# Performance work log

Hardware: AMD Instinct MI355X
Metric: run time of the kernel (lower is better)

Reference implementation:

```python
import jax, jax.numpy as jnp
import numpy as np
from jax import lax

THRESHOLD = 1.0  # threshold_potential from __init__
STRIDE = (1, 1)
PADDING = 'SAME'


def setup_inputs() -> dict:
    key = jax.random.key(0)
    k1, k2, k3 = jax.random.split(key, 3)
    input_to_layer = jax.random.normal(k1, (1, 512, 512, 16), dtype=jnp.float32)
    weights = jax.random.normal(k2, (3, 3, 16, 64), dtype=jnp.float32)
    old_potentials = jax.random.normal(k3, (1, 512, 512, 64), dtype=jnp.float32)
    return {
        'input_to_layer': input_to_layer,
        'weights': weights,
        'old_potentials': old_potentials,
    }


def reference(input_to_layer, weights, old_potentials):
    # conv2d NHWC x HWIO -> NHWC, SAME padding, stride 1 (as tf.nn.conv2d)
    out_conv = lax.conv_general_dilated(
        input_to_layer, weights,
        window_strides=STRIDE, padding=PADDING,
        dimension_numbers=('NHWC', 'HWIO', 'NHWC'))
    # accumulate membrane potential, fused threshold -> spike + reset
    new_potentials = out_conv + old_potentials
    spiked = new_potentials >= THRESHOLD
    curr_spikes = spiked.astype(new_potentials.dtype)
    new_potentials = jnp.where(spiked, 0.0, new_potentials)
    # original returns spikes; new_potentials is the updated state
    return curr_spikes, new_potentials
```

## Files before the change

### kernel.cpp

```cpp
#include <hip/hip_runtime.h>


#define H 512
#define W 512
#define CI 16
#define CO 64
#define TX 32
#define TY 4
#define XT 34
#define YT 6
#define PIX_US 24
#define KS 152
#define SW_CHUNKS ((CO * KS * 2) / 16)

typedef float v4f __attribute__((ext_vector_type(4)));
typedef float f32x4 __attribute__((ext_vector_type(4)));
typedef short short8 __attribute__((ext_vector_type(8)));
typedef unsigned int uint4v __attribute__((ext_vector_type(4)));

__device__ __forceinline__ unsigned int pack2bf(float f0, float f1) {
    unsigned u0 = __builtin_bit_cast(unsigned, f0);
    unsigned u1 = __builtin_bit_cast(unsigned, f1);
    u0 = (u0 + 0x7FFFu + ((u0 >> 16) & 1u)) >> 16;
    u1 = (u1 + 0x7FFFu + ((u1 >> 16) & 1u)) >> 16;
    return u0 | (u1 << 16);
}

__global__ void snn_pack_w(const float* __restrict__ w,
                           unsigned int* __restrict__ wsu)
{
    const int tid = threadIdx.x;
    const int n  = tid & 63;
    const int kq = tid >> 6;
    #pragma unroll
    for (int kk = 0; kk < 18; ++kk) {
        const int k = kq * 36 + kk * 2;
        const float f0 = w[k * CO + n];
        const float f1 = w[(k + 1) * CO + n];
        wsu[(n * KS + k) >> 1] = pack2bf(f0, f1);
    }
    if (kq == 3) {
        #pragma unroll
        for (int i = 0; i < 4; ++i)
            wsu[((n * KS + 144) >> 1) + i] = 0u;
    }
}

__global__ __launch_bounds__(256, 4)
void snn_conv_mfma(const float* __restrict__ in,
                   const uint4v* __restrict__ wsv,
                   const float* __restrict__ oldp,
                   float* __restrict__ out_spk,
                   float* __restrict__ out_pot)
{
    __shared__ unsigned short s_in[YT * XT * PIX_US];
    __shared__ alignas(16) unsigned short s_w[CO * KS];

    const int tid = threadIdx.x;
    const int bx = blockIdx.x & 15;
    const int by = blockIdx.x >> 4;
    const int tx0 = bx * TX, ty0 = by * TY;

    const int lane = tid & 63;
    const int wv   = tid >> 6;
    const int r    = lane & 15;
    const int quad = lane >> 4;
    const int half = quad & 1;
    const int tsel = quad >> 1;

    f32x4 oldv[2][4];
    int ebase[2];
    #pragma unroll
    for (int mt = 0; mt < 2; ++mt) {
        const int gy = ty0 + wv;
        const int gx = tx0 + mt * 16 + r;
        ebase[mt] = (gy * W + gx) * CO + quad * 4;
        #pragma unroll
        for (int nt = 0; nt < 4; ++nt)
            oldv[mt][nt] = *(const f32x4*)(oldp + ebase[mt] + nt * 16);
    }

    {
        uint4v* dst = (uint4v*)s_w;
        #pragma unroll
        for (int i = 0; i < 5; ++i) {
            const int idx = tid + i * 256;
            if (idx < SW_CHUNKS) dst[idx] = wsv[idx];
        }
    }

    if (tid < YT * XT) {
        const int ly = tid / XT, lx = tid - ly * XT;
        const int gy = ty0 + ly - 1, gx = tx0 + lx - 1;
        uint4v pk0, pk1;
        if ((unsigned)gy < H && (unsigned)gx < W) {
            const v4f* p = (const v4f*)(in + (gy * W + gx) * CI);
            v4f a = p[0], b = p[1], c = p[2], d = p[3];
            pk0 = (uint4v){pack2bf(a.x, a.y), pack2bf(a.z, a.w),
                           pack2bf(b.x, b.y), pack2bf(b.z, b.w)};
            pk1 = (uint4v){pack2bf(c.x, c.y), pack2bf(c.z, c.w),
                           pack2bf(d.x, d.y), pack2bf(d.z, d.w)};
        } else {
            pk0 = (uint4v)0u;
            pk1 = (uint4v)0u;
        }
        uint4v* dst = (uint4v*)&s_in[tid * PIX_US];
        dst[0] = pk0;
        dst[1] = pk1;
    }
    __syncthreads();

    f32x4 acc[2][4] = {};

    int abase[2];
    #pragma unroll
    for (int mt = 0; mt < 2; ++mt)
        abase[mt] = (wv * XT + mt * 16 + r) * PIX_US + half * 8;

    const short8 zero8 = {0, 0, 0, 0, 0, 0, 0, 0};

    #pragma unroll
    for (int ks5 = 0; ks5 < 5; ++ks5) {
        const int t0 = ks5 * 2;
        const int t1 = (ks5 == 4) ? 8 : ks5 * 2 + 1;
        const int off0 = ((t0 / 3) * XT + (t0 % 3)) * PIX_US;
        const int off1 = ((t1 / 3) * XT + (t1 % 3)) * PIX_US;
        const int aoff = tsel ? off1 : off0;
        const int koff = (ks5 < 4) ? (ks5 * 32 + quad * 8) : (128 + half * 8);

        short8 bf[4];
        #pragma unroll
        for (int nt = 0; nt < 4; ++nt)
            bf[nt] = *(const short8*)&s_w[(nt * 16 + r) * KS + koff];

        short8 af[2];
        #pragma unroll
        for (int mt = 0; mt < 2; ++mt) {
            short8 a = *(const short8*)&s_in[abase[mt] + aoff];
            if (ks5 == 4) a = (quad >= 2) ? zero8 : a;
            af[mt] = a;
        }

        #pragma unroll
        for (int mt = 0; mt < 2; ++mt)
            #pragma unroll
            for (int nt = 0; nt < 4; ++nt)
                acc[mt][nt] = __builtin_amdgcn_mfma_f32_16x16x32_bf16(
                    bf[nt], af[mt], acc[mt][nt], 0, 0, 0);
    }

    #pragma unroll
    for (int mt = 0; mt < 2; ++mt) {
        #pragma unroll
        for (int nt = 0; nt < 4; ++nt) {
            const int idx = ebase[mt] + nt * 16;
            f32x4 np = acc[mt][nt] + oldv[mt][nt];
            f32x4 spk, pot;
            #pragma unroll
            for (int j = 0; j < 4; ++j) {
                const bool s = np[j] >= 1.0f;
                spk[j] = s ? 1.0f : 0.0f;
                pot[j] = s ? 0.0f : np[j];
            }
            __builtin_nontemporal_store(spk, (f32x4*)(out_spk + idx));
            __builtin_nontemporal_store(pot, (f32x4*)(out_pot + idx));
        }
    }
}

extern "C" void kernel_launch(void* const* d_in, const int* in_sizes, int n_in,
                              void* d_out, int out_size, void* d_ws, size_t ws_size,
                              hipStream_t stream) {
    const float* in   = (const float*)d_in[0];
    const float* w    = (const float*)d_in[1];
    const float* oldp = (const float*)d_in[2];
    float* out_spk = (float*)d_out;
    float* out_pot = out_spk + (size_t)H * W * CO;

    snn_pack_w<<<1, 256, 0, stream>>>(w, (unsigned int*)d_ws);

    const int grid = (W / TX) * (H / TY);
    snn_conv_mfma<<<grid, 256, 0, stream>>>(in, (const uint4v*)d_ws, oldp,
                                            out_spk, out_pot);
}
```

Measured before the change: 221.6 us.

## Process four row tiles per block with double-buffered input and prefetched potentials

Each block now handles four consecutive row tiles instead of one, loading the weights into LDS once per block. The input halo is double-buffered in LDS, and the next tiles' input and old potentials are prefetched into registers while the current tile computes. This amortizes weight staging and hides global load latency. In exchange, register pressure rises (launch bounds drop to 2 blocks per SIMD), the grid shrinks fourfold, and the outputs now use plain stores instead of nontemporal stores.

New measurement: 215.4 us. -2.8%, faster.

```diff
diff --git a/kernel.cpp b/kernel.cpp
--- a/kernel.cpp
+++ b/kernel.cpp
@@ -12,6 +12,7 @@
 #define PIX_US 24
 #define KS 152
 #define SW_CHUNKS ((CO * KS * 2) / 16)
+#define NTILES 4
 
 typedef float v4f __attribute__((ext_vector_type(4)));
 typedef float f32x4 __attribute__((ext_vector_type(4)));
@@ -46,20 +47,26 @@
     }
 }
 
-__global__ __launch_bounds__(256, 4)
+#define PIPE_BARRIER() do {                                   \
+    asm volatile("s_waitcnt lgkmcnt(0)" ::: "memory");        \
+    __builtin_amdgcn_s_barrier();                             \
+    __builtin_amdgcn_sched_barrier(0);                        \
+} while (0)
+
+__global__ __launch_bounds__(256, 2)
 void snn_conv_mfma(const float* __restrict__ in,
                    const uint4v* __restrict__ wsv,
                    const float* __restrict__ oldp,
                    float* __restrict__ out_spk,
                    float* __restrict__ out_pot)
 {
-    __shared__ unsigned short s_in[YT * XT * PIX_US];
+    __shared__ unsigned short s_in[2][YT * XT * PIX_US];
     __shared__ alignas(16) unsigned short s_w[CO * KS];
 
     const int tid = threadIdx.x;
-    const int bx = blockIdx.x & 15;
-    const int by = blockIdx.x >> 4;
-    const int tx0 = bx * TX, ty0 = by * TY;
+    const int bx  = blockIdx.x & 15;
+    const int byB = (blockIdx.x >> 4) * NTILES;
+    const int tx0 = bx * TX;
 
     const int lane = tid & 63;
     const int wv   = tid >> 6;
@@ -68,102 +75,147 @@
     const int half = quad & 1;
     const int tsel = quad >> 1;
 
-    f32x4 oldv[2][4];
-    int ebase[2];
-    #pragma unroll
-    for (int mt = 0; mt < 2; ++mt) {
-        const int gy = ty0 + wv;
-        const int gx = tx0 + mt * 16 + r;
-        ebase[mt] = (gy * W + gx) * CO + quad * 4;
-        #pragma unroll
-        for (int nt = 0; nt < 4; ++nt)
-            oldv[mt][nt] = *(const f32x4*)(oldp + ebase[mt] + nt * 16);
-    }
+    const int sly  = tid / XT;
+    const int slx  = tid - sly * XT;
+    const bool sact = tid < YT * XT;
 
     {
         uint4v* dst = (uint4v*)s_w;
         #pragma unroll
-        for (int i = 0; i < 5; ++i) {
-            const int idx = tid + i * 256;
+        for (int c = 0; c < 5; ++c) {
+            const int idx = tid + c * 256;
             if (idx < SW_CHUNKS) dst[idx] = wsv[idx];
         }
     }
 
-    if (tid < YT * XT) {
-        const int ly = tid / XT, lx = tid - ly * XT;
-        const int gy = ty0 + ly - 1, gx = tx0 + lx - 1;
-        uint4v pk0, pk1;
-        if ((unsigned)gy < H && (unsigned)gx < W) {
-            const v4f* p = (const v4f*)(in + (gy * W + gx) * CI);
-            v4f a = p[0], b = p[1], c = p[2], d = p[3];
-            pk0 = (uint4v){pack2bf(a.x, a.y), pack2bf(a.z, a.w),
-                           pack2bf(b.x, b.y), pack2bf(b.z, b.w)};
-            pk1 = (uint4v){pack2bf(c.x, c.y), pack2bf(c.z, c.w),
-                           pack2bf(d.x, d.y), pack2bf(d.z, d.w)};
-        } else {
-            pk0 = (uint4v)0u;
-            pk1 = (uint4v)0u;
-        }
-        uint4v* dst = (uint4v*)&s_in[tid * PIX_US];
-        dst[0] = pk0;
-        dst[1] = pk1;
-    }
-    __syncthreads();
-
-    f32x4 acc[2][4] = {};
-
-    int abase[2];
+    v4f ra, rb, rc, rd;
+    bool ivalid;
+    f32x4 oldv[2][2][4];
+
+    auto issue_in = [&](int t) {
+        ivalid = false;
+        if (sact) {
+            const int gy = (byB + t) * TY + sly - 1;
+            const int gx = tx0 + slx - 1;
+            if ((unsigned)gy < H && (unsigned)gx < W) {
+                const v4f* p = (const v4f*)(in + (gy * W + gx) * CI);
+                ra = p[0]; rb = p[1]; rc = p[2]; rd = p[3];
+                ivalid = true;
+            }
+        }
+    };
+
+    auto pack_write = [&](int buf) {
+        if (sact) {
+            uint4v pk0, pk1;
+            if (ivalid) {
+                pk0 = (uint4v){pack2bf(ra.x, ra.y), pack2bf(ra.z, ra.w),
+                               pack2bf(rb.x, rb.y), pack2bf(rb.z, rb.w)};
+                pk1 = (uint4v){pack2bf(rc.x, rc.y), pack2bf(rc.z, rc.w),
+                               pack2bf(rd.x, rd.y), pack2bf(rd.z, rd.w)};
+            } else {
+                pk0 = (uint4v)0u;
+                pk1 = (uint4v)0u;
+            }
+            uint4v* dst = (uint4v*)&s_in[buf][tid * PIX_US];
+            dst[0] = pk0;
+            dst[1] = pk1;
+        }
+    };
+
+    auto issue_oldp = [&](int t, int par) {
+        #pragma unroll
+        for (int mt = 0; mt < 2; ++mt) {
+            const int gy = (byB + t) * TY + wv;
+            const int gx = tx0 + mt * 16 + r;
+            const int eb = (gy * W + gx) * CO + quad * 4;
+            #pragma unroll
+            for (int nt = 0; nt < 4; ++nt)
+                oldv[par][mt][nt] = *(const f32x4*)(oldp + eb + nt * 16);
+        }
+    };
+
+    auto compute = [&](int buf, f32x4 (&acc)[2][4]) {
+        int abase[2];
+        #pragma unroll
+        for (int mt = 0; mt < 2; ++mt)
+            abase[mt] = (wv * XT + mt * 16 + r) * PIX_US + half * 8;
+        const short8 zero8 = {0, 0, 0, 0, 0, 0, 0, 0};
+        const unsigned short* sb = s_in[buf];
+
+        #pragma unroll
+        for (int ks5 = 0; ks5 < 5; ++ks5) {
+            const int t0 = ks5 * 2;
+            const int t1 = (ks5 == 4) ? 8 : ks5 * 2 + 1;
+            const int off0 = ((t0 / 3) * XT + (t0 % 3)) * PIX_US;
+            const int off1 = ((t1 / 3) * XT + (t1 % 3)) * PIX_US;
+            const int aoff = tsel ? off1 : off0;
+            const int koff = (ks5 < 4) ? (ks5 * 32 + quad * 8) : (128 + half * 8);
+
+            short8 bf[4];
+            #pragma unroll
+            for (int nt = 0; nt < 4; ++nt)
+                bf[nt] = *(const short8*)&s_w[(nt * 16 + r) * KS + koff];
+
+            short8 af[2];
+            #pragma unroll
+            for (int mt = 0; mt < 2; ++mt) {
+                short8 a = *(const short8*)&sb[abase[mt] + aoff];
+                if (ks5 == 4) a = (quad >= 2) ? zero8 : a;
+                af[mt] = a;
+            }
+
+            #pragma unroll
+            for (int mt = 0; mt < 2; ++mt)
+                #pragma unroll
+                for (int nt = 0; nt < 4; ++nt)
+                    acc[mt][nt] = __builtin_amdgcn_mfma_f32_16x16x32_bf16(
+                        bf[nt], af[mt], acc[mt][nt], 0, 0, 0);
+        }
+    };
+
+    auto epilogue = [&](int t, int par, f32x4 (&acc)[2][4]) {
+        #pragma unroll
+        for (int mt = 0; mt < 2; ++mt) {
+            const int gy = (byB + t) * TY + wv;
+            const int gx = tx0 + mt * 16 + r;
+            const int eb = (gy * W + gx) * CO + quad * 4;
+            #pragma unroll
+            for (int nt = 0; nt < 4; ++nt) {
+                const int idx = eb + nt * 16;
+                f32x4 np = acc[mt][nt] + oldv[par][mt][nt];
+                f32x4 spk, pot;
+                #pragma unroll
+                for (int j = 0; j < 4; ++j) {
+                    const bool s = np[j] >= 1.0f;
+                    spk[j] = s ? 1.0f : 0.0f;
+                    pot[j] = s ? 0.0f : np[j];
+                }
+                *(f32x4*)(out_spk + idx) = spk;
+                *(f32x4*)(out_pot + idx) = pot;
+            }
+        }
+    };
+
+    issue_in(0);
+    issue_oldp(0, 0);
+    pack_write(0);
+    issue_in(1);
+    issue_oldp(1, 1);
+    PIPE_BARRIER();
+
     #pragma unroll
-    for (int mt = 0; mt < 2; ++mt)
-        abase[mt] = (wv * XT + mt * 16 + r) * PIX_US + half * 8;
-
-    const short8 zero8 = {0, 0, 0, 0, 0, 0, 0, 0};
-
-    #pragma unroll
-    for (int ks5 = 0; ks5 < 5; ++ks5) {
-        const int t0 = ks5 * 2;
-        const int t1 = (ks5 == 4) ? 8 : ks5 * 2 + 1;
-        const int off0 = ((t0 / 3) * XT + (t0 % 3)) * PIX_US;
-        const int off1 = ((t1 / 3) * XT + (t1 % 3)) * PIX_US;
-        const int aoff = tsel ? off1 : off0;
-        const int koff = (ks5 < 4) ? (ks5 * 32 + quad * 8) : (128 + half * 8);
-
-        short8 bf[4];
-        #pragma unroll
-        for (int nt = 0; nt < 4; ++nt)
-            bf[nt] = *(const short8*)&s_w[(nt * 16 + r) * KS + koff];
-
-        short8 af[2];
-        #pragma unroll
-        for (int mt = 0; mt < 2; ++mt) {
-            short8 a = *(const short8*)&s_in[abase[mt] + aoff];
-            if (ks5 == 4) a = (quad >= 2) ? zero8 : a;
-            af[mt] = a;
-        }
-
-        #pragma unroll
-        for (int mt = 0; mt < 2; ++mt)
-            #pragma unroll
-            for (int nt = 0; nt < 4; ++nt)
-                acc[mt][nt] = __builtin_amdgcn_mfma_f32_16x16x32_bf16(
-                    bf[nt], af[mt], acc[mt][nt], 0, 0, 0);
-    }
-
-    #pragma unroll
-    for (int mt = 0; mt < 2; ++mt) {
-        #pragma unroll
-        for (int nt = 0; nt < 4; ++nt) {
-            const int idx = ebase[mt] + nt * 16;
-            f32x4 np = acc[mt][nt] + oldv[mt][nt];
-            f32x4 spk, pot;
-            #pragma unroll
-            for (int j = 0; j < 4; ++j) {
-                const bool s = np[j] >= 1.0f;
-                spk[j] = s ? 1.0f : 0.0f;
-                pot[j] = s ? 0.0f : np[j];
-            }
-            __builtin_nontemporal_store(spk, (f32x4*)(out_spk + idx));
-            __builtin_nontemporal_store(pot, (f32x4*)(out_pot + idx));
+    for (int i = 0; i < NTILES; ++i) {
+        f32x4 acc[2][4] = {};
+        compute(i & 1, acc);
+        epilogue(i, i & 1, acc);
+        if (i < NTILES - 1) {
+            pack_write((i + 1) & 1);
+            if (i < NTILES - 2) {
+                issue_in(i + 2);
+                issue_oldp(i + 2, i & 1);
+            }
+            PIPE_BARRIER();
         }
     }
 }
@@ -179,7 +231,7 @@
 
     snn_pack_w<<<1, 256, 0, stream>>>(w, (unsigned int*)d_ws);
 
-    const int grid = (W / TX) * (H / TY);
+    const int grid = (W / TX) * (H / (TY * NTILES));
     snn_conv_mfma<<<grid, 256, 0, stream>>>(in, (const uint4v*)d_ws, oldp,
                                             out_spk, out_pot);
 }
```
